# Kernel tuning notes

Hardware: AMD Instinct MI355X
Metric: run time of the kernel (lower is better)

Reference implementation:

```python
import jax, jax.numpy as jnp
import numpy as np
from jax import lax

N, K, T_OBS, PRED = 64, 48, 30, 15
EMB, NODE, EDGE, ATT, CNN = 64, 128, 256, 64, 512


def setup_inputs():
    key = jax.random.key(0)
    ks = jax.random.split(key, 18)
    rn = lambda k, s, sc=1.0: jax.random.normal(k, s, jnp.float32) * sc
    return {
        "img_embedding": rn(ks[0], (N, CNN)),
        "target_obs_pos_abs": rn(ks[1], (N, T_OBS, 2)),
        "target_obs_pos_rel": rn(ks[2], (N, T_OBS, 2)),
        "target_obs_pos_step": rn(ks[3], (N, T_OBS, 2), 0.1),
        "nearby_obs_pos_abs": rn(ks[4], (N, K, T_OBS, 2)),
        "nearby_obs_pos_rel": rn(ks[5], (N, K, T_OBS, 2)),
        "nearby_obs_pos_step": rn(ks[6], (N, K, T_OBS, 2), 0.1),
        "target_obs_hist_size": jax.random.randint(ks[7], (N, 1), 0, T_OBS),
        "nearby_obs_hist_sizes": jax.random.randint(ks[8], (N, K, 1), 0, T_OBS),
        "W_disp": rn(ks[9], (EMB, 2), 0.1), "b_disp": jnp.zeros((EMB,), jnp.float32),
        "Wih_t": rn(ks[10], (4 * NODE, EMB), 0.05), "Whh_t": rn(ks[11], (4 * NODE, NODE), 0.05),
        "bih_t": jnp.zeros((4 * NODE,), jnp.float32), "bhh_t": jnp.zeros((4 * NODE,), jnp.float32),
        "Wih_n": rn(ks[12], (4 * EDGE, EMB), 0.05), "Whh_n": rn(ks[13], (4 * EDGE, EDGE), 0.05),
        "bih_n": jnp.zeros((4 * EDGE,), jnp.float32), "bhh_n": jnp.zeros((4 * EDGE,), jnp.float32),
        "W_att_t": rn(ks[14], (ATT, 2), 0.1), "b_att_t": jnp.zeros((ATT,), jnp.float32),
        "W_att_n": rn(ks[15], (ATT, 2), 0.1), "b_att_n": jnp.zeros((ATT,), jnp.float32),
        "W_pred": rn(ks[16], (2, NODE + CNN + EDGE), 0.02), "b_pred": jnp.zeros((2,), jnp.float32),
    }


def _lstm_cell(x, h, c, Wih, Whh, bih, bhh):
    # PyTorch LSTM gate order: i, f, g, o
    g = x @ Wih.T + h @ Whh.T + bih + bhh
    i, f, gg, o = jnp.split(g, 4, axis=-1)
    c2 = jax.nn.sigmoid(f) * c + jax.nn.sigmoid(i) * jnp.tanh(gg)
    return jax.nn.sigmoid(o) * jnp.tanh(c2), c2


def _forward(img_embedding, target_obs_pos_abs, target_obs_pos_rel, target_obs_pos_step,
             nearby_obs_pos_abs, nearby_obs_pos_rel, nearby_obs_pos_step,
             W_disp, b_disp, Wih_t, Whh_t, bih_t, bhh_t, Wih_n, Whh_n, bih_n, bhh_n,
             W_att_t, b_att_t, W_att_n, b_att_n, W_pred, b_pred,
             target_obs_hist_size, nearby_obs_hist_sizes):
    t_hist = target_obs_hist_size[:, 0]          # [N]
    n_hist = nearby_obs_hist_sizes[:, :, 0]      # [N, K]
    M = N * K

    def step(carry, t):
        tht, tct, nht, nct, Ht, cabs, crel, cstep, nabs, nstep = carry
        is_obs = t < T_OBS
        tc = jnp.minimum(t, T_OBS - 1)
        # prediction branch (only takes effect when t >= T_OBS)
        pred_out = jnp.concatenate([tht, img_embedding, Ht], 1) @ W_pred.T + b_pred  # [N,2]
        cabs = jnp.where(is_obs, target_obs_pos_abs[:, tc], cabs + pred_out)
        crel = jnp.where(is_obs, target_obs_pos_rel[:, tc], crel + pred_out)
        cstep = jnp.where(is_obs, target_obs_pos_step[:, tc], pred_out)
        nabs = jnp.where(is_obs, nearby_obs_pos_abs[:, :, tc], nabs)
        nstep = jnp.where(is_obs, nearby_obs_pos_step[:, :, tc], nstep)
        tmask = jnp.where(is_obs, t_hist > T_OBS - t, True)   # [N] bool
        nmask = jnp.where(is_obs, n_hist > T_OBS - t, True)   # [N,K] bool
        gate_t = jnp.sum(tmask) > 0  # emulates 'continue' when no target observed
        # target LSTM step, masked scatter-back
        th2, tc2 = _lstm_cell(cstep @ W_disp.T + b_disp, tht, tct, Wih_t, Whh_t, bih_t, bhh_t)
        u = (tmask & gate_t)[:, None]
        tht = jnp.where(u, th2, tht)
        tct = jnp.where(u, tc2, tct)
        # nearby LSTM step, masked scatter-back
        currN = jnp.sum(nmask)
        gate_n = gate_t & (currN > 0)
        nh2, nc2 = _lstm_cell(nstep.reshape(M, 2) @ W_disp.T + b_disp, nht, nct, Wih_n, Whh_n, bih_n, bhh_n)
        un = (nmask.reshape(M) & gate_n)[:, None]
        nht = jnp.where(un, nh2, nht)
        nct = jnp.where(un, nc2, nct)
        # social attention over padded nearby dim
        an = (nabs - cabs[:, None, :]) @ W_att_n.T + b_att_n   # [N,K,ATT]
        at = crel @ W_att_t.T + b_att_t                        # [N,ATT]
        mf = nmask.astype(jnp.float32)
        sc = jnp.einsum('nka,na->nk', an, at) * currN.astype(jnp.float32) / jnp.sqrt(jnp.float32(ATT))
        sc = sc * mf
        num = jnp.exp(sc - jnp.max(sc, 1, keepdims=True)) * mf
        w = num / (jnp.sum(num, 1, keepdims=True) + 1e-6)
        Ht = jnp.where(gate_n, jnp.einsum('nke,nk->ne', nht.reshape(N, K, EDGE), w), Ht)
        return (tht, tct, nht, nct, Ht, cabs, crel, cstep, nabs, nstep), crel

    z = lambda s: jnp.zeros(s, jnp.float32)
    init = (z((N, NODE)), z((N, NODE)), z((M, EDGE)), z((M, EDGE)), z((N, EDGE)),
            z((N, 2)), z((N, 2)), z((N, 2)), z((N, K, 2)), z((N, K, 2)))
    _, rels = lax.scan(step, init, jnp.arange(1, T_OBS + PRED))
    # last PRED emitted crel values are pred_traj[:, 0:PRED]
    return jnp.transpose(rels[-PRED:], (1, 0, 2))


def reference(img_embedding, target_obs_pos_abs, target_obs_pos_rel, target_obs_pos_step,
              nearby_obs_pos_abs, nearby_obs_pos_rel, nearby_obs_pos_step,
              target_obs_hist_size, nearby_obs_hist_sizes,
              W_disp, b_disp, Wih_t, Whh_t, bih_t, bhh_t, Wih_n, Whh_n, bih_n, bhh_n,
              W_att_t, b_att_t, W_att_n, b_att_n, W_pred, b_pred):
    return _forward(img_embedding, target_obs_pos_abs, target_obs_pos_rel, target_obs_pos_step,
                    nearby_obs_pos_abs, nearby_obs_pos_rel, nearby_obs_pos_step,
                    W_disp, b_disp, Wih_t, Whh_t, bih_t, bhh_t, Wih_n, Whh_n, bih_n, bhh_n,
                    W_att_t, b_att_t, W_att_n, b_att_n, W_pred, b_pred,
                    target_obs_hist_size, nearby_obs_hist_sizes)
```

## Files before the change

kernel.cpp:

```cpp
#include <hip/hip_runtime.h>
#include <math.h>

#define NT 64
#define KN 48
#define TOBS 30
#define NPRED 15
#define EMB 64
#define NODE 128
#define EDGE 256
#define ATTD 64
#define CNN 512
#define GNN 1024
#define GTT 512
#define TMAX 44

typedef _Float16 f16;
typedef f16 f16x8 __attribute__((ext_vector_type(8)));
typedef f16 f16x2 __attribute__((ext_vector_type(2)));
typedef float f32x4 __attribute__((ext_vector_type(4)));

__device__ __forceinline__ float rcp_f(float x) { return __builtin_amdgcn_rcpf(x); }
__device__ __forceinline__ float sigm(float x) { return rcp_f(1.f + __expf(-x)); }
__device__ __forceinline__ float tanh_f(float x) {
  float xx = fminf(fmaxf(x, -20.f), 20.f);
  float e = __expf(-2.f * xx);
  return (1.f - e) * rcp_f(1.f + e);
}
__device__ __forceinline__ unsigned ldcoh(const unsigned* p) {
  return __hip_atomic_load(p, __ATOMIC_RELAXED, __HIP_MEMORY_SCOPE_AGENT);
}
__device__ __forceinline__ unsigned long long ldcoh8(const unsigned long long* p) {
  return __hip_atomic_load(p, __ATOMIC_RELAXED, __HIP_MEMORY_SCOPE_AGENT);
}
__device__ __forceinline__ float ldcohf(const float* p) {
  unsigned u = __hip_atomic_load((const unsigned*)p, __ATOMIC_RELAXED, __HIP_MEMORY_SCOPE_AGENT);
  return __builtin_bit_cast(float, u);
}
__device__ __forceinline__ void stcoh(unsigned* p, unsigned v) {
  __hip_atomic_store(p, v, __ATOMIC_RELAXED, __HIP_MEMORY_SCOPE_AGENT);
}
__device__ __forceinline__ void stcohf(float* p, float v) {
  __hip_atomic_store((unsigned*)p, __builtin_bit_cast(unsigned, v),
                     __ATOMIC_RELAXED, __HIP_MEMORY_SCOPE_AGENT);
}

__global__ __launch_bounds__(512) void prep_kernel(
    const float* __restrict__ Wih_n, const float* __restrict__ Whh_n,
    const float* __restrict__ bih_n, const float* __restrict__ bhh_n,
    const float* __restrict__ Wih_t, const float* __restrict__ Whh_t,
    const float* __restrict__ bih_t, const float* __restrict__ bhh_t,
    const float* __restrict__ W_disp, const float* __restrict__ b_disp,
    const int* __restrict__ t_hist, const int* __restrict__ n_hist,
    f16* __restrict__ Wn, f16* __restrict__ Wt,
    float* __restrict__ Ptv, float* __restrict__ Pnv,
    float* __restrict__ bias_n, float* __restrict__ bias_t,
    int* __restrict__ gt_arr, int* __restrict__ gn_arr, float* __restrict__ cn_arr,
    int* __restrict__ last29p, unsigned* __restrict__ flags)
{
  const int gid = blockIdx.x * 512 + threadIdx.x;
  const int nthr = gridDim.x * 512;
  __shared__ int sgn[TMAX + 1];

  if (gid < 2 * NT) flags[gid] = 0u;

  for (int idx = gid; idx < GNN * 288; idx += nthr) {
    const int j    = idx & 7;
    const int lane = (idx >> 3) & 63;
    const int g    = (idx >> 9) & 3;
    const int r    = idx >> 11;
    const int u    = r % 9;
    const int s    = r / 9;
    const int w    = s & 7;
    const int h    = s >> 3;
    const int col = g * 256 + h * 128 + w * 16 + (lane & 15);
    float v = 0.f;
    if (u > 0) {
      const int k = (u - 1) * 32 + (lane >> 4) * 8 + j;
      v = Whh_n[col * EDGE + k];
    }
    Wn[idx] = (f16)v;
  }
  for (int idx = gid; idx < GTT * 192; idx += nthr) {
    const int j = idx & 7;
    const int col = (idx >> 3) & 511;
    const int c8 = idx >> 12;
    const int k = c8 * 8 + j;
    const float v = (k < EMB) ? Wih_t[col * EMB + k] : Whh_t[col * NODE + (k - EMB)];
    Wt[idx] = (f16)v;
  }
  for (int idx = gid; idx < 3 * GTT; idx += nthr) {
    const int sel = idx / GTT;
    const int col = idx - sel * GTT;
    float acc = 0.f;
    for (int e = 0; e < EMB; ++e) {
      const float sv = (sel == 0) ? W_disp[e * 2]
                     : (sel == 1) ? W_disp[e * 2 + 1] : b_disp[e];
      acc += sv * Wih_t[col * EMB + e];
    }
    Ptv[sel * GTT + col] = acc;
  }
  for (int idx = gid; idx < 3 * GNN; idx += nthr) {
    const int sel = idx / GNN;
    const int col = idx - sel * GNN;
    float acc = 0.f;
    for (int e = 0; e < EMB; ++e) {
      const float sv = (sel == 0) ? W_disp[e * 2]
                     : (sel == 1) ? W_disp[e * 2 + 1] : b_disp[e];
      acc += sv * Wih_n[col * EMB + e];
    }
    Pnv[sel * GNN + col] = acc;
  }
  for (int idx = gid; idx < GNN; idx += nthr) bias_n[idx] = bih_n[idx] + bhh_n[idx];
  for (int idx = gid; idx < GTT; idx += nthr) bias_t[idx] = bih_t[idx] + bhh_t[idx];

  if (blockIdx.x == 0 && threadIdx.x < 352) {
    const int t = (threadIdx.x >> 3) + 1;
    const int part = threadIdx.x & 7;
    int any_t = 0, cnt = 0;
    if (t < TOBS) {
      const int thr = TOBS - t;
      for (int nn = part; nn < NT; nn += 8) any_t |= (t_hist[nn] > thr) ? 1 : 0;
      for (int m = part; m < NT * KN; m += 8) cnt += (n_hist[m] > thr) ? 1 : 0;
    } else { any_t = (part == 0); cnt = (part == 0) ? NT * KN : 0; }
    #pragma unroll
    for (int off = 1; off < 8; off <<= 1) {
      any_t |= __shfl_xor(any_t, off);
      cnt   += __shfl_xor(cnt, off);
    }
    if (part == 0) {
      const int gn = (any_t && cnt > 0) ? 1 : 0;
      gt_arr[t] = any_t;
      gn_arr[t] = gn;
      cn_arr[t] = (float)cnt;
      sgn[t] = gn;
    }
  }
  __syncthreads();
  if (blockIdx.x == 0 && threadIdx.x == 0) {
    int l = 30;
    for (int t = 29; t >= 1; --t) if (sgn[t]) { l = t; break; }
    last29p[0] = l;
  }
}

__global__ __launch_bounds__(512, 2) void model_kernel(
    const float* __restrict__ img, const float* __restrict__ tabs,
    const float* __restrict__ trel, const float* __restrict__ tstep,
    const float* __restrict__ nabs_g, const float* __restrict__ nstep_g,
    const int* __restrict__ thist_g, const int* __restrict__ nhist_g,
    const float* __restrict__ W_att_t, const float* __restrict__ b_att_t,
    const float* __restrict__ W_att_n, const float* __restrict__ b_att_n,
    const float* __restrict__ W_pred, const float* __restrict__ b_pred,
    const f16* __restrict__ Wn, const f16* __restrict__ Wt,
    const float* __restrict__ Ptv, const float* __restrict__ Pnv,
    const float* __restrict__ bias_n, const float* __restrict__ bias_t,
    const int* __restrict__ gt_arr, const int* __restrict__ gn_arr,
    const float* __restrict__ cn_arr, const int* __restrict__ last29p,
    unsigned* __restrict__ flags, unsigned* __restrict__ Hglob,
    float* __restrict__ Tglob,
    float* __restrict__ out)
{
  __shared__ f16 s_wlds[3 * 16384];
  __shared__ float s_step[KN][2];
  __shared__ f16 Ah[KN][264];
  __shared__ float s_tht[NODE];
  __shared__ float s_tct[64];
  __shared__ f16  s_th16[NODE];
  __shared__ float s_Ht[EDGE];
  __shared__ float s_g[256];
  __shared__ float s_bt[256];
  __shared__ float s_sc[KN], s_w[KN];
  __shared__ float s_scal[8];
  __shared__ float s_dd[4];
  __shared__ float s_pimg[2];
  __shared__ int   s_nh[KN];
  __shared__ float s_wp[2][384];
  __shared__ float s_wan0[ATTD], s_wan1[ATTD], s_ban[ATTD];
  __shared__ float s_wat0[ATTD], s_wat1[ATTD], s_bat[ATTD];

  const int tid  = threadIdx.x;
  const int n    = blockIdx.x & 63;
  const int hb   = blockIdx.x >> 6;
  const int w    = tid >> 6;
  const int lane = tid & 63;
  const int cl   = lane & 15;
  const int kq   = lane >> 4;
  const int koff = kq * 8;

  for (int i = tid; i < KN * 264; i += 512) ((f16*)Ah)[i] = (f16)0.f;
  if (tid < KN * 2) ((float*)s_step)[tid] = 0.f;
  for (int i = tid; i < NODE; i += 512) { s_tht[i] = 0.f; s_th16[i] = (f16)0.f; }
  if (tid < 64) s_tct[tid] = 0.f;
  for (int i = tid; i < EDGE; i += 512) s_Ht[i] = 0.f;
  if (tid < 256) {
    const int g = tid >> 6, dl = tid & 63;
    s_bt[tid] = bias_t[g * 128 + hb * 64 + dl];
  }
  for (int i = tid; i < 768; i += 512) {
    const int ww = i / 384, j = i - ww * 384;
    s_wp[ww][j] = (j < 128) ? W_pred[ww * 896 + j] : W_pred[ww * 896 + 640 + (j - 128)];
  }
  if (tid < KN) s_nh[tid] = nhist_g[n * KN + tid];
  if (tid < 8) s_scal[tid] = 0.f;
  if (tid >= 64 && tid < 128) {
    const int a = tid - 64;
    s_wan0[a] = W_att_n[a * 2]; s_wan1[a] = W_att_n[a * 2 + 1]; s_ban[a] = b_att_n[a];
  }
  if (tid >= 128 && tid < 192) {
    const int a = tid - 128;
    s_wat0[a] = W_att_t[a * 2]; s_wat1[a] = W_att_t[a * 2 + 1]; s_bat[a] = b_att_t[a];
  }
  const int thist = thist_g[n];
  const int last29 = last29p[0];

  float pt0 = 0.f, pt1 = 0.f, ptb = 0.f;
  if (tid < 256) {
    const int col = (tid >> 6) * 128 + hb * 64 + (tid & 63);
    pt0 = Ptv[col]; pt1 = Ptv[512 + col]; ptb = Ptv[1024 + col];
  }

  const int e_g = hb * 128 + w * 16 + cl;

  float pn0[4], pn1[4], bias_q[4];
  #pragma unroll
  for (int g = 0; g < 4; ++g) {
    const int col = g * 256 + e_g;
    pn0[g] = Pnv[col];
    pn1[g] = Pnv[1024 + col];
    bias_q[g] = bias_n[col] + Pnv[2048 + col];
  }

  for (int i = tid; i < 3 * 8 * 256; i += 512) {
    const int c  = i & 255;
    const int wv = (i >> 8) & 7;
    const int sl = i >> 11;
    const size_t gbase = ((size_t)((hb * 8 + wv) * 9 + (sl + 1))) * 2048;
    *(f16x8*)(s_wlds + (size_t)(sl * 8 + wv) * 2048 + c * 8) =
        *(const f16x8*)(Wn + gbase + c * 8);
  }

  if (w < 2) {
    float s = 0.f;
    for (int j = lane; j < CNN; j += 64) s += img[n * CNN + j] * W_pred[w * 896 + 128 + j];
    for (int off = 32; off; off >>= 1) s += __shfl_down(s, off);
    if (lane == 0) s_pimg[w] = s + b_pred[w];
  }

  float creg[3][4];
  #pragma unroll
  for (int b = 0; b < 3; ++b)
    #pragma unroll
    for (int c = 0; c < 4; ++c) creg[b][c] = 0.f;

  const f16* gW = Wn + ((size_t)(hb * 8 + w) * 9) * 2048 + (size_t)lane * 8;
  const f16* lW = s_wlds + (size_t)w * 2048 + (size_t)lane * 8;
  unsigned* myflag = flags + n * 2 + hb;
  unsigned* otflag = flags + n * 2 + (1 - hb);
  int bn = 0;

  __syncthreads();

  {
    if (tid < 96) {
      const int row = tid >> 1, comp = tid & 1;
      s_step[row][comp] = nstep_g[((n * KN + row) * TOBS + 1) * 2 + comp];
    }
    if (tid < 2) {
      s_scal[tid]     = tabs[(n * TOBS + 1) * 2 + tid];
      s_scal[2 + tid] = trel[(n * TOBS + 1) * 2 + tid];
      s_scal[4 + tid] = tstep[(n * TOBS + 1) * 2 + tid];
    }
    if (tid >= 384 && tid < 448) {
      const int a = tid - 384;
      const float r0 = trel[(n * TOBS + 1) * 2 + 0], r1 = trel[(n * TOBS + 1) * 2 + 1];
      const float at = r0 * s_wat0[a] + r1 * s_wat1[a] + s_bat[a];
      float p0 = at * s_wan0[a], p1 = at * s_wan1[a], pb = at * s_ban[a];
      #pragma unroll
      for (int off = 32; off; off >>= 1) {
        p0 += __shfl_xor(p0, off); p1 += __shfl_xor(p1, off); pb += __shfl_xor(pb, off);
      }
      if (a == 0) { s_dd[0] = p0; s_dd[1] = p1; s_dd[2] = pb; }
    }
  }
  __syncthreads();

  for (int t = 1; t <= TMAX; ++t) {
    const bool is_obs = (t < TOBS);
    const int tc = is_obs ? t : (TOBS - 1);
    const int gate_t = gt_arr[t];
    const int gate_n = gn_arr[t];
    const float currN = cn_arr[t];
    const bool tmask = is_obs ? (thist > (TOBS - t)) : true;
    const bool do_t = gate_t && tmask;
    const bool need_x = (gate_n || do_t);
    const bool do_att = gate_n && (t >= last29);
    const int par = bn & 1;

    if (!is_obs) {
      if (w < 2) {
        float s = 0.f;
        for (int j = lane; j < NODE; j += 64) s += s_tht[j] * s_wp[w][j];
        for (int j = lane; j < EDGE; j += 64) s += s_Ht[j] * s_wp[w][128 + j];
        for (int off = 32; off; off >>= 1) s += __shfl_down(s, off);
        if (lane == 0) {
          const float p = s + s_pimg[w];
          const float cabs = s_scal[w] + p;
          const float crel = s_scal[2 + w] + p;
          s_scal[w] = cabs; s_scal[2 + w] = crel; s_scal[4 + w] = p;
          if (hb == 0) out[(n * NPRED + (t - TOBS)) * 2 + w] = crel;
        }
      }
      __syncthreads();
      if (tid >= 384 && tid < 448) {
        const int a = tid - 384;
        const float at = s_scal[2] * s_wat0[a] + s_scal[3] * s_wat1[a] + s_bat[a];
        float p0 = at * s_wan0[a], p1 = at * s_wan1[a], pb = at * s_ban[a];
        #pragma unroll
        for (int off = 32; off; off >>= 1) {
          p0 += __shfl_xor(p0, off); p1 += __shfl_xor(p1, off); pb += __shfl_xor(pb, off);
        }
        if (a == 0) { s_dd[0] = p0; s_dd[1] = p1; s_dd[2] = pb; }
      }
      __syncthreads();
    }

    f16 hreg[3][4];
    if (gate_n) {
      f32x4 acc[3][4];
      #pragma unroll
      for (int rt = 0; rt < 3; ++rt)
        #pragma unroll
        for (int g = 0; g < 4; ++g) acc[rt][g] = (f32x4){0.f, 0.f, 0.f, 0.f};

      #pragma unroll
      for (int u = 1; u <= 8; ++u) {
        f16x8 bf[4];
        if (u <= 3) {
          #pragma unroll
          for (int g = 0; g < 4; ++g)
            bf[g] = *(const f16x8*)(lW + (u - 1) * 16384 + g * 512);
        } else {
          #pragma unroll
          for (int g = 0; g < 4; ++g)
            bf[g] = *(const f16x8*)(gW + u * 2048 + g * 512);
        }
        f16x8 af[3];
        #pragma unroll
        for (int rt = 0; rt < 3; ++rt) {
          const int row = rt * 16 + cl;
          af[rt] = *(const f16x8*)&Ah[row][(u - 1) * 32 + koff];
        }
        #pragma unroll
        for (int g = 0; g < 4; ++g)
          #pragma unroll
          for (int rt = 0; rt < 3; ++rt)
            acc[rt][g] = __builtin_amdgcn_mfma_f32_16x16x32_f16(af[rt], bf[g], acc[rt][g], 0, 0, 0);
      }

      unsigned* Hg = Hglob + (size_t)(par * NT + n) * (KN * 128);
      #pragma unroll
      for (int rt = 0; rt < 3; ++rt) {
        #pragma unroll
        for (int jj = 0; jj < 4; ++jj) {
          const int row = rt * 16 + kq * 4 + jj;
          const bool nm = is_obs ? (s_nh[row] > (TOBS - t)) : true;
          f16 hv;
          if (nm) {
            const float s0 = s_step[row][0], s1 = s_step[row][1];
            const float iv = acc[rt][0][jj] + bias_q[0] + s0 * pn0[0] + s1 * pn1[0];
            const float fv = acc[rt][1][jj] + bias_q[1] + s0 * pn0[1] + s1 * pn1[1];
            const float gv = acc[rt][2][jj] + bias_q[2] + s0 * pn0[2] + s1 * pn1[2];
            const float ov = acc[rt][3][jj] + bias_q[3] + s0 * pn0[3] + s1 * pn1[3];
            const float c2 = sigm(fv) * creg[rt][jj] + sigm(iv) * tanh_f(gv);
            creg[rt][jj] = c2;
            hv = (f16)(sigm(ov) * tanh_f(c2));
          } else {
            hv = Ah[row][e_g];
          }
          hreg[rt][jj] = hv;
          const unsigned lo = (unsigned)__builtin_bit_cast(unsigned short, hv);
          const unsigned hi = (unsigned)__shfl_down((int)lo, 1);
          if (!(cl & 1))
            stcoh(Hg + row * 128 + (e_g >> 1), lo | (hi << 16));
        }
      }
    }

    if (do_t && tid < 256) {
      float g0 = s_bt[tid] + s_scal[4] * pt0 + s_scal[5] * pt1 + ptb;
      float g1 = 0.f, g2 = 0.f, g3 = 0.f;
      const f16x2* th2 = (const f16x2*)s_th16;
      const f16x8* wp = (const f16x8*)(Wt + ((tid >> 6) * 128 + hb * 64 + (tid & 63)) * 8);
      #pragma unroll
      for (int c8 = 0; c8 < 16; ++c8) {
        const f16x8 wv = wp[(c8 + 8) * 512];
        f16x2 w0 = {wv[0], wv[1]}, w1 = {wv[2], wv[3]};
        f16x2 w2 = {wv[4], wv[5]}, w3 = {wv[6], wv[7]};
        g0 = __builtin_amdgcn_fdot2(w0, th2[c8 * 4 + 0], g0, false);
        g1 = __builtin_amdgcn_fdot2(w1, th2[c8 * 4 + 1], g1, false);
        g2 = __builtin_amdgcn_fdot2(w2, th2[c8 * 4 + 2], g2, false);
        g3 = __builtin_amdgcn_fdot2(w3, th2[c8 * 4 + 3], g3, false);
      }
      s_g[tid] = (g0 + g1) + (g2 + g3);
    }
    if (do_att && tid >= 256 && tid < 256 + KN) {
      const int k = tid - 256;
      const float a0 = nabs_g[((n * KN + k) * TOBS + tc) * 2 + 0] - s_scal[0];
      const float a1 = nabs_g[((n * KN + k) * TOBS + tc) * 2 + 1] - s_scal[1];
      const bool nm = is_obs ? (s_nh[k] > (TOBS - t)) : true;
      const float sc = (a0 * s_dd[0] + a1 * s_dd[1] + s_dd[2]) * currN * 0.125f;
      s_sc[k] = nm ? sc : 0.f;
      s_w[k]  = nm ? 1.f : 0.f;
    }
    __syncthreads();

    if (do_t && tid < 64) {
      const int d = hb * 64 + tid;
      const float iv = s_g[tid], fv = s_g[64 + tid];
      const float gv = s_g[128 + tid], ov = s_g[192 + tid];
      const float c2 = sigm(fv) * s_tct[tid] + sigm(iv) * tanh_f(gv);
      s_tct[tid] = c2;
      const float nh = sigm(ov) * tanh_f(c2);
      s_tht[d] = nh;
      s_th16[d] = (f16)nh;
      stcohf(Tglob + ((size_t)(par * NT + n) * 2 + hb) * 64 + tid, nh);
    }
    if (do_att && w == 4) {
      const bool act = lane < KN;
      const float sc = act ? s_sc[lane] : -1.0e30f;
      const float mf = act ? s_w[lane] : 0.f;
      float mx = sc;
      #pragma unroll
      for (int off = 32; off; off >>= 1) mx = fmaxf(mx, __shfl_xor(mx, off));
      float num = __expf(sc - mx) * mf;
      float sum = num;
      #pragma unroll
      for (int off = 32; off; off >>= 1) sum += __shfl_xor(sum, off);
      if (act) s_w[lane] = num * rcp_f(sum + 1e-6f);
    }
    __syncthreads();

    if (need_x && tid == 0) {
      stcoh(myflag, (unsigned)(bn + 1));
    }

    if (gate_n) {
      #pragma unroll
      for (int rt = 0; rt < 3; ++rt)
        #pragma unroll
        for (int jj = 0; jj < 4; ++jj)
          Ah[rt * 16 + kq * 4 + jj][e_g] = hreg[rt][jj];
    }

    {
      const int tn = t + 1;
      if (tn <= TOBS) {
        const int tcn = (tn < TOBS) ? tn : (TOBS - 1);
        if (tid < 96) {
          const int row = tid >> 1, comp = tid & 1;
          s_step[row][comp] = nstep_g[((n * KN + row) * TOBS + tcn) * 2 + comp];
        }
      }
      if (tn < TOBS) {
        if (tid < 2) {
          s_scal[tid]     = tabs[(n * TOBS + tn) * 2 + tid];
          s_scal[2 + tid] = trel[(n * TOBS + tn) * 2 + tid];
          s_scal[4 + tid] = tstep[(n * TOBS + tn) * 2 + tid];
        }
        if (tid >= 384 && tid < 448) {
          const int a = tid - 384;
          const float r0 = trel[(n * TOBS + tn) * 2 + 0], r1 = trel[(n * TOBS + tn) * 2 + 1];
          const float at = r0 * s_wat0[a] + r1 * s_wat1[a] + s_bat[a];
          float p0 = at * s_wan0[a], p1 = at * s_wan1[a], pb = at * s_ban[a];
          #pragma unroll
          for (int off = 32; off; off >>= 1) {
            p0 += __shfl_xor(p0, off); p1 += __shfl_xor(p1, off); pb += __shfl_xor(pb, off);
          }
          if (a == 0) { s_dd[0] = p0; s_dd[1] = p1; s_dd[2] = pb; }
        }
      }
    }

    if (need_x && tid == 0) {
      const unsigned step = (unsigned)(bn + 1);
      while (ldcoh(otflag) < step)
        __builtin_amdgcn_s_sleep(1);
    }
    __syncthreads();

    if (gate_n) {
      const unsigned long long* Hg8 =
          (const unsigned long long*)(Hglob + (size_t)(par * NT + n) * (KN * 128));
      const int ob8 = (1 - hb) * 32;
      for (int i = tid; i < KN * 32; i += 512) {
        const int row = i >> 5, c = i & 31;
        const unsigned long long v = ldcoh8(Hg8 + row * 64 + ob8 + c);
        *(unsigned long long*)&Ah[row][((1 - hb) * 64 + c * 2) * 2] = v;
      }
    }
    if (do_t && tid >= 448) {
      const int dl = tid - 448;
      const int d = (1 - hb) * 64 + dl;
      const float nh = ldcohf(Tglob + ((size_t)(par * NT + n) * 2 + (1 - hb)) * 64 + dl);
      s_tht[d] = nh;
      s_th16[d] = (f16)nh;
    }
    __syncthreads();

    if (do_att && tid < EDGE) {
      float h0 = 0.f, h1 = 0.f, h2 = 0.f, h3 = 0.f;
      #pragma unroll
      for (int k = 0; k < KN; k += 4) {
        h0 += (float)Ah[k][tid]     * s_w[k];
        h1 += (float)Ah[k + 1][tid] * s_w[k + 1];
        h2 += (float)Ah[k + 2][tid] * s_w[k + 2];
        h3 += (float)Ah[k + 3][tid] * s_w[k + 3];
      }
      s_Ht[tid] = (h0 + h1) + (h2 + h3);
    }
    if (need_x) bn++;
    if (t >= 29) __syncthreads();
  }
}

extern "C" void kernel_launch(void* const* d_in, const int* in_sizes, int n_in,
                              void* d_out, int out_size, void* d_ws, size_t ws_size,
                              hipStream_t stream) {
  const float* img    = (const float*)d_in[0];
  const float* tabs   = (const float*)d_in[1];
  const float* trel   = (const float*)d_in[2];
  const float* tstep  = (const float*)d_in[3];
  const float* nabs   = (const float*)d_in[4];
  const float* nstep  = (const float*)d_in[6];
  const int*   thist  = (const int*)d_in[7];
  const int*   nhist  = (const int*)d_in[8];
  const float* W_disp = (const float*)d_in[9];
  const float* b_disp = (const float*)d_in[10];
  const float* Wih_t  = (const float*)d_in[11];
  const float* Whh_t  = (const float*)d_in[12];
  const float* bih_t  = (const float*)d_in[13];
  const float* bhh_t  = (const float*)d_in[14];
  const float* Wih_n  = (const float*)d_in[15];
  const float* Whh_n  = (const float*)d_in[16];
  const float* bih_n  = (const float*)d_in[17];
  const float* bhh_n  = (const float*)d_in[18];
  const float* W_att_t = (const float*)d_in[19];
  const float* b_att_t = (const float*)d_in[20];
  const float* W_att_n = (const float*)d_in[21];
  const float* b_att_n = (const float*)d_in[22];
  const float* W_pred  = (const float*)d_in[23];
  const float* b_pred  = (const float*)d_in[24];

  char* ws = (char*)d_ws;
  f16*      Wn      = (f16*)(ws);
  f16*      Wt      = (f16*)(ws + 655360);
  float*    bias_n  = (float*)(ws + 851968);
  float*    bias_t  = (float*)(ws + 856064);
  int*      gt_arr  = (int*)(ws + 858112);
  int*      gn_arr  = (int*)(ws + 858304);
  float*    cn_arr  = (float*)(ws + 858496);
  int*      last29p = (int*)(ws + 859648);
  unsigned* flags   = (unsigned*)(ws + 860160);
  float*    Ptv     = (float*)(ws + 901120);
  float*    Pnv     = (float*)(ws + 917504);
  unsigned* Hglob   = (unsigned*)(ws + 1048576);
  float*    Tglob   = (float*)(ws + 4194304);

  prep_kernel<<<64, 512, 0, stream>>>(Wih_n, Whh_n, bih_n, bhh_n, Wih_t, Whh_t,
                                      bih_t, bhh_t, W_disp, b_disp,
                                      thist, nhist, Wn, Wt, Ptv, Pnv,
                                      bias_n, bias_t, gt_arr, gn_arr, cn_arr,
                                      last29p, flags);
  model_kernel<<<2 * NT, 512, 0, stream>>>(img, tabs, trel, tstep, nabs, nstep,
                                           thist, nhist,
                                           W_att_t, b_att_t, W_att_n, b_att_n,
                                           W_pred, b_pred,
                                           Wn, Wt, Ptv, Pnv, bias_n, bias_t,
                                           gt_arr, gn_arr, cn_arr, last29p,
                                           flags, Hglob, Tglob,
                                           (float*)d_out);
}
```

Baseline: 616.4 us.

## Replace block barriers with LDS counter signaling and double-buffer per-step scalars

Removes two __syncthreads per timestep. Each wave now increments an LDS counter once its global stores have drained, and a single thread waits on that counter before publishing the cross-block flag. The target LSTM cell update is moved into per-wave registers using shuffles instead of the s_g/s_tct shared arrays, and the attention score and softmax are merged into one wave. Step, scalar and dd buffers are double-buffered so the next step's prefetch does not race with current readers, and the remote H loads are issued before the local Ah writes to overlap their latency. This adds subtle ordering risk around the spin-wait and the parity buffers.

After: 632.1 us. +2.5%, slower.

```diff
diff --git a/kernel.cpp b/kernel.cpp
--- a/kernel.cpp
+++ b/kernel.cpp
@@ -161,22 +161,21 @@
     float* __restrict__ out)
 {
   __shared__ f16 s_wlds[3 * 16384];
-  __shared__ float s_step[KN][2];
+  __shared__ float s_step[2][KN][2];
   __shared__ f16 Ah[KN][264];
   __shared__ float s_tht[NODE];
-  __shared__ float s_tct[64];
+  __shared__ float s_tct_unused;
   __shared__ f16  s_th16[NODE];
   __shared__ float s_Ht[EDGE];
-  __shared__ float s_g[256];
-  __shared__ float s_bt[256];
-  __shared__ float s_sc[KN], s_w[KN];
-  __shared__ float s_scal[8];
-  __shared__ float s_dd[4];
+  __shared__ float s_w[KN];
+  __shared__ float s_scal[2][8];
+  __shared__ float s_dd[2][4];
   __shared__ float s_pimg[2];
   __shared__ int   s_nh[KN];
   __shared__ float s_wp[2][384];
   __shared__ float s_wan0[ATTD], s_wan1[ATTD], s_ban[ATTD];
   __shared__ float s_wat0[ATTD], s_wat1[ATTD], s_bat[ATTD];
+  __shared__ int   s_cnt;
 
   const int tid  = threadIdx.x;
   const int n    = blockIdx.x & 63;
@@ -188,20 +187,17 @@
   const int koff = kq * 8;
 
   for (int i = tid; i < KN * 264; i += 512) ((f16*)Ah)[i] = (f16)0.f;
-  if (tid < KN * 2) ((float*)s_step)[tid] = 0.f;
+  for (int i = tid; i < 2 * KN * 2; i += 512) ((float*)s_step)[i] = 0.f;
   for (int i = tid; i < NODE; i += 512) { s_tht[i] = 0.f; s_th16[i] = (f16)0.f; }
-  if (tid < 64) s_tct[tid] = 0.f;
   for (int i = tid; i < EDGE; i += 512) s_Ht[i] = 0.f;
-  if (tid < 256) {
-    const int g = tid >> 6, dl = tid & 63;
-    s_bt[tid] = bias_t[g * 128 + hb * 64 + dl];
-  }
+  if (tid < 16) ((float*)s_scal)[tid] = 0.f;
+  if (tid < 8) ((float*)s_dd)[tid] = 0.f;
+  if (tid == 0) s_cnt = 0;
   for (int i = tid; i < 768; i += 512) {
     const int ww = i / 384, j = i - ww * 384;
     s_wp[ww][j] = (j < 128) ? W_pred[ww * 896 + j] : W_pred[ww * 896 + 640 + (j - 128)];
   }
   if (tid < KN) s_nh[tid] = nhist_g[n * KN + tid];
-  if (tid < 8) s_scal[tid] = 0.f;
   if (tid >= 64 && tid < 128) {
     const int a = tid - 64;
     s_wan0[a] = W_att_n[a * 2]; s_wan1[a] = W_att_n[a * 2 + 1]; s_ban[a] = b_att_n[a];
@@ -213,13 +209,16 @@
   const int thist = thist_g[n];
   const int last29 = last29p[0];
 
-  float pt0 = 0.f, pt1 = 0.f, ptb = 0.f;
-  if (tid < 256) {
-    const int col = (tid >> 6) * 128 + hb * 64 + (tid & 63);
-    pt0 = Ptv[col]; pt1 = Ptv[512 + col]; ptb = Ptv[1024 + col];
-  }
-
   const int e_g = hb * 128 + w * 16 + cl;
+
+  const int dr = lane & 15;
+  const int dcol = (lane >> 4) * 128 + hb * 64 + w * 16 + dr;
+  float btreg = 0.f, ptd0 = 0.f, ptd1 = 0.f, ptdb = 0.f;
+  if (w < 4) {
+    btreg = bias_t[dcol];
+    ptd0 = Ptv[dcol]; ptd1 = Ptv[512 + dcol]; ptdb = Ptv[1024 + dcol];
+  }
+  float tctreg = 0.f, nhreg = 0.f;
 
   float pn0[4], pn1[4], bias_q[4];
   #pragma unroll
@@ -257,18 +256,19 @@
   unsigned* myflag = flags + n * 2 + hb;
   unsigned* otflag = flags + n * 2 + (1 - hb);
   int bn = 0;
+  int tgt = 0;
 
   __syncthreads();
 
   {
     if (tid < 96) {
       const int row = tid >> 1, comp = tid & 1;
-      s_step[row][comp] = nstep_g[((n * KN + row) * TOBS + 1) * 2 + comp];
+      s_step[1][row][comp] = nstep_g[((n * KN + row) * TOBS + 1) * 2 + comp];
     }
     if (tid < 2) {
-      s_scal[tid]     = tabs[(n * TOBS + 1) * 2 + tid];
-      s_scal[2 + tid] = trel[(n * TOBS + 1) * 2 + tid];
-      s_scal[4 + tid] = tstep[(n * TOBS + 1) * 2 + tid];
+      s_scal[1][tid]     = tabs[(n * TOBS + 1) * 2 + tid];
+      s_scal[1][2 + tid] = trel[(n * TOBS + 1) * 2 + tid];
+      s_scal[1][4 + tid] = tstep[(n * TOBS + 1) * 2 + tid];
     }
     if (tid >= 384 && tid < 448) {
       const int a = tid - 384;
@@ -279,12 +279,13 @@
       for (int off = 32; off; off >>= 1) {
         p0 += __shfl_xor(p0, off); p1 += __shfl_xor(p1, off); pb += __shfl_xor(pb, off);
       }
-      if (a == 0) { s_dd[0] = p0; s_dd[1] = p1; s_dd[2] = pb; }
+      if (a == 0) { s_dd[1][0] = p0; s_dd[1][1] = p1; s_dd[1][2] = pb; }
     }
   }
   __syncthreads();
 
   for (int t = 1; t <= TMAX; ++t) {
+    tgt += 8;
     const bool is_obs = (t < TOBS);
     const int tc = is_obs ? t : (TOBS - 1);
     const int gate_t = gt_arr[t];
@@ -295,6 +296,8 @@
     const bool need_x = (gate_n || do_t);
     const bool do_att = gate_n && (t >= last29);
     const int par = bn & 1;
+    const int ps = is_obs ? (t & 1) : 1;
+    const int pp = (t <= TOBS) ? (t & 1) : 0;
 
     if (!is_obs) {
       if (w < 2) {
@@ -304,22 +307,22 @@
         for (int off = 32; off; off >>= 1) s += __shfl_down(s, off);
         if (lane == 0) {
           const float p = s + s_pimg[w];
-          const float cabs = s_scal[w] + p;
-          const float crel = s_scal[2 + w] + p;
-          s_scal[w] = cabs; s_scal[2 + w] = crel; s_scal[4 + w] = p;
+          const float cabs = s_scal[ps][w] + p;
+          const float crel = s_scal[ps][2 + w] + p;
+          s_scal[ps][w] = cabs; s_scal[ps][2 + w] = crel; s_scal[ps][4 + w] = p;
           if (hb == 0) out[(n * NPRED + (t - TOBS)) * 2 + w] = crel;
         }
       }
       __syncthreads();
       if (tid >= 384 && tid < 448) {
         const int a = tid - 384;
-        const float at = s_scal[2] * s_wat0[a] + s_scal[3] * s_wat1[a] + s_bat[a];
+        const float at = s_scal[ps][2] * s_wat0[a] + s_scal[ps][3] * s_wat1[a] + s_bat[a];
         float p0 = at * s_wan0[a], p1 = at * s_wan1[a], pb = at * s_ban[a];
         #pragma unroll
         for (int off = 32; off; off >>= 1) {
           p0 += __shfl_xor(p0, off); p1 += __shfl_xor(p1, off); pb += __shfl_xor(pb, off);
         }
-        if (a == 0) { s_dd[0] = p0; s_dd[1] = p1; s_dd[2] = pb; }
+        if (a == 0) { s_dd[ps][0] = p0; s_dd[ps][1] = p1; s_dd[ps][2] = pb; }
       }
       __syncthreads();
     }
@@ -366,7 +369,7 @@
           const bool nm = is_obs ? (s_nh[row] > (TOBS - t)) : true;
           f16 hv;
           if (nm) {
-            const float s0 = s_step[row][0], s1 = s_step[row][1];
+            const float s0 = s_step[pp][row][0], s1 = s_step[pp][row][1];
             const float iv = acc[rt][0][jj] + bias_q[0] + s0 * pn0[0] + s1 * pn1[0];
             const float fv = acc[rt][1][jj] + bias_q[1] + s0 * pn0[1] + s1 * pn1[1];
             const float gv = acc[rt][2][jj] + bias_q[2] + s0 * pn0[2] + s1 * pn1[2];
@@ -386,86 +389,80 @@
       }
     }
 
-    if (do_t && tid < 256) {
-      float g0 = s_bt[tid] + s_scal[4] * pt0 + s_scal[5] * pt1 + ptb;
-      float g1 = 0.f, g2 = 0.f, g3 = 0.f;
-      const f16x2* th2 = (const f16x2*)s_th16;
-      const f16x8* wp = (const f16x8*)(Wt + ((tid >> 6) * 128 + hb * 64 + (tid & 63)) * 8);
-      #pragma unroll
-      for (int c8 = 0; c8 < 16; ++c8) {
-        const f16x8 wv = wp[(c8 + 8) * 512];
-        f16x2 w0 = {wv[0], wv[1]}, w1 = {wv[2], wv[3]};
-        f16x2 w2 = {wv[4], wv[5]}, w3 = {wv[6], wv[7]};
-        g0 = __builtin_amdgcn_fdot2(w0, th2[c8 * 4 + 0], g0, false);
-        g1 = __builtin_amdgcn_fdot2(w1, th2[c8 * 4 + 1], g1, false);
-        g2 = __builtin_amdgcn_fdot2(w2, th2[c8 * 4 + 2], g2, false);
-        g3 = __builtin_amdgcn_fdot2(w3, th2[c8 * 4 + 3], g3, false);
-      }
-      s_g[tid] = (g0 + g1) + (g2 + g3);
-    }
-    if (do_att && tid >= 256 && tid < 256 + KN) {
-      const int k = tid - 256;
-      const float a0 = nabs_g[((n * KN + k) * TOBS + tc) * 2 + 0] - s_scal[0];
-      const float a1 = nabs_g[((n * KN + k) * TOBS + tc) * 2 + 1] - s_scal[1];
-      const bool nm = is_obs ? (s_nh[k] > (TOBS - t)) : true;
-      const float sc = (a0 * s_dd[0] + a1 * s_dd[1] + s_dd[2]) * currN * 0.125f;
-      s_sc[k] = nm ? sc : 0.f;
-      s_w[k]  = nm ? 1.f : 0.f;
-    }
-    __syncthreads();
-
-    if (do_t && tid < 64) {
-      const int d = hb * 64 + tid;
-      const float iv = s_g[tid], fv = s_g[64 + tid];
-      const float gv = s_g[128 + tid], ov = s_g[192 + tid];
-      const float c2 = sigm(fv) * s_tct[tid] + sigm(iv) * tanh_f(gv);
-      s_tct[tid] = c2;
-      const float nh = sigm(ov) * tanh_f(c2);
-      s_tht[d] = nh;
-      s_th16[d] = (f16)nh;
-      stcohf(Tglob + ((size_t)(par * NT + n) * 2 + hb) * 64 + tid, nh);
-    }
-    if (do_att && w == 4) {
-      const bool act = lane < KN;
-      const float sc = act ? s_sc[lane] : -1.0e30f;
-      const float mf = act ? s_w[lane] : 0.f;
-      float mx = sc;
-      #pragma unroll
-      for (int off = 32; off; off >>= 1) mx = fmaxf(mx, __shfl_xor(mx, off));
-      float num = __expf(sc - mx) * mf;
-      float sum = num;
-      #pragma unroll
-      for (int off = 32; off; off >>= 1) sum += __shfl_xor(sum, off);
-      if (act) s_w[lane] = num * rcp_f(sum + 1e-6f);
-    }
-    __syncthreads();
-
-    if (need_x && tid == 0) {
-      stcoh(myflag, (unsigned)(bn + 1));
-    }
-
-    if (gate_n) {
-      #pragma unroll
-      for (int rt = 0; rt < 3; ++rt)
-        #pragma unroll
-        for (int jj = 0; jj < 4; ++jj)
-          Ah[rt * 16 + kq * 4 + jj][e_g] = hreg[rt][jj];
+    if (w < 4) {
+      if (do_t) {
+        const f16x2* th2 = (const f16x2*)s_th16;
+        const f16x8* wpd = (const f16x8*)(Wt + dcol * 8);
+        float g0 = btreg + s_scal[ps][4] * ptd0 + s_scal[ps][5] * ptd1 + ptdb;
+        float g1 = 0.f, g2 = 0.f, g3 = 0.f;
+        #pragma unroll
+        for (int c8 = 0; c8 < 16; ++c8) {
+          const f16x8 wv = wpd[(c8 + 8) * 512];
+          f16x2 w0 = {wv[0], wv[1]}, w1 = {wv[2], wv[3]};
+          f16x2 w2 = {wv[4], wv[5]}, w3 = {wv[6], wv[7]};
+          g0 = __builtin_amdgcn_fdot2(w0, th2[c8 * 4 + 0], g0, false);
+          g1 = __builtin_amdgcn_fdot2(w1, th2[c8 * 4 + 1], g1, false);
+          g2 = __builtin_amdgcn_fdot2(w2, th2[c8 * 4 + 2], g2, false);
+          g3 = __builtin_amdgcn_fdot2(w3, th2[c8 * 4 + 3], g3, false);
+        }
+        const float gg = (g0 + g1) + (g2 + g3);
+        const float gi = __shfl(gg, dr);
+        const float gf = __shfl(gg, 16 + dr);
+        const float gG = __shfl(gg, 32 + dr);
+        const float go = __shfl(gg, 48 + dr);
+        if (lane < 16) {
+          const float c2 = sigm(gf) * tctreg + sigm(gi) * tanh_f(gG);
+          tctreg = c2;
+          nhreg = sigm(go) * tanh_f(c2);
+          stcohf(Tglob + ((size_t)(par * NT + n) * 2 + hb) * 64 + (w * 16 + dr), nhreg);
+        }
+      }
+      asm volatile("s_waitcnt vmcnt(0)" ::: "memory");
+      if (lane == 0) atomicAdd(&s_cnt, 1);
+    } else {
+      asm volatile("s_waitcnt vmcnt(0)" ::: "memory");
+      if (lane == 0) atomicAdd(&s_cnt, 1);
+      if (w == 4 && do_att) {
+        float sc = -1.0e30f, mf = 0.f;
+        if (lane < KN) {
+          const float a0 = nabs_g[((n * KN + lane) * TOBS + tc) * 2 + 0] - s_scal[ps][0];
+          const float a1 = nabs_g[((n * KN + lane) * TOBS + tc) * 2 + 1] - s_scal[ps][1];
+          const bool nm = is_obs ? (s_nh[lane] > (TOBS - t)) : true;
+          sc = nm ? (a0 * s_dd[ps][0] + a1 * s_dd[ps][1] + s_dd[ps][2]) * currN * 0.125f : 0.f;
+          mf = nm ? 1.f : 0.f;
+        }
+        float mx = sc;
+        #pragma unroll
+        for (int off = 32; off; off >>= 1) mx = fmaxf(mx, __shfl_xor(mx, off));
+        float num = __expf(sc - mx) * mf;
+        float sum = num;
+        #pragma unroll
+        for (int off = 32; off; off >>= 1) sum += __shfl_xor(sum, off);
+        if (lane < KN) s_w[lane] = num * rcp_f(sum + 1e-6f);
+      }
+      if (w == 5 && lane == 0 && need_x) {
+        while (__hip_atomic_load(&s_cnt, __ATOMIC_RELAXED, __HIP_MEMORY_SCOPE_WORKGROUP) < tgt)
+          __builtin_amdgcn_s_sleep(1);
+        asm volatile("" ::: "memory");
+        stcoh(myflag, (unsigned)(bn + 1));
+      }
     }
 
     {
       const int tn = t + 1;
+      const int q = tn & 1;
       if (tn <= TOBS) {
         const int tcn = (tn < TOBS) ? tn : (TOBS - 1);
         if (tid < 96) {
           const int row = tid >> 1, comp = tid & 1;
-          s_step[row][comp] = nstep_g[((n * KN + row) * TOBS + tcn) * 2 + comp];
+          s_step[q][row][comp] = nstep_g[((n * KN + row) * TOBS + tcn) * 2 + comp];
         }
       }
       if (tn < TOBS) {
         if (tid < 2) {
-          s_scal[tid]     = tabs[(n * TOBS + tn) * 2 + tid];
-          s_scal[2 + tid] = trel[(n * TOBS + tn) * 2 + tid];
-          s_scal[4 + tid] = tstep[(n * TOBS + tn) * 2 + tid];
+          s_scal[q][tid]     = tabs[(n * TOBS + tn) * 2 + tid];
+          s_scal[q][2 + tid] = trel[(n * TOBS + tn) * 2 + tid];
+          s_scal[q][4 + tid] = tstep[(n * TOBS + tn) * 2 + tid];
         }
         if (tid >= 384 && tid < 448) {
           const int a = tid - 384;
@@ -476,27 +473,39 @@
           for (int off = 32; off; off >>= 1) {
             p0 += __shfl_xor(p0, off); p1 += __shfl_xor(p1, off); pb += __shfl_xor(pb, off);
           }
-          if (a == 0) { s_dd[0] = p0; s_dd[1] = p1; s_dd[2] = pb; }
-        }
-      }
-    }
-
-    if (need_x && tid == 0) {
+          if (a == 0) { s_dd[q][0] = p0; s_dd[q][1] = p1; s_dd[q][2] = pb; }
+        }
+      }
+    }
+
+    if (need_x && tid == 320) {
       const unsigned step = (unsigned)(bn + 1);
       while (ldcoh(otflag) < step)
         __builtin_amdgcn_s_sleep(1);
     }
     __syncthreads();
 
+    unsigned long long pv0 = 0, pv1 = 0, pv2 = 0;
+    const int pr = tid >> 5, pc = tid & 31;
     if (gate_n) {
       const unsigned long long* Hg8 =
           (const unsigned long long*)(Hglob + (size_t)(par * NT + n) * (KN * 128));
       const int ob8 = (1 - hb) * 32;
-      for (int i = tid; i < KN * 32; i += 512) {
-        const int row = i >> 5, c = i & 31;
-        const unsigned long long v = ldcoh8(Hg8 + row * 64 + ob8 + c);
-        *(unsigned long long*)&Ah[row][((1 - hb) * 64 + c * 2) * 2] = v;
-      }
+      pv0 = ldcoh8(Hg8 + (pr)      * 64 + ob8 + pc);
+      pv1 = ldcoh8(Hg8 + (pr + 16) * 64 + ob8 + pc);
+      pv2 = ldcoh8(Hg8 + (pr + 32) * 64 + ob8 + pc);
+    }
+    if (gate_n) {
+      #pragma unroll
+      for (int rt = 0; rt < 3; ++rt)
+        #pragma unroll
+        for (int jj = 0; jj < 4; ++jj)
+          Ah[rt * 16 + kq * 4 + jj][e_g] = hreg[rt][jj];
+    }
+    if (do_t && w < 4 && lane < 16) {
+      const int d = hb * 64 + w * 16 + dr;
+      s_tht[d] = nhreg;
+      s_th16[d] = (f16)nhreg;
     }
     if (do_t && tid >= 448) {
       const int dl = tid - 448;
@@ -504,6 +513,12 @@
       const float nh = ldcohf(Tglob + ((size_t)(par * NT + n) * 2 + (1 - hb)) * 64 + dl);
       s_tht[d] = nh;
       s_th16[d] = (f16)nh;
+    }
+    if (gate_n) {
+      const int cb = ((1 - hb) * 64 + pc * 2) * 2;
+      *(unsigned long long*)&Ah[pr][cb]      = pv0;
+      *(unsigned long long*)&Ah[pr + 16][cb] = pv1;
+      *(unsigned long long*)&Ah[pr + 32][cb] = pv2;
     }
     __syncthreads();
 
@@ -519,7 +534,7 @@
       s_Ht[tid] = (h0 + h1) + (h2 + h3);
     }
     if (need_x) bn++;
-    if (t >= 29) __syncthreads();
+    if (t >= 29 || t + 1 >= last29) __syncthreads();
   }
 }
 
```
